# Kernel tuning notes

Hardware: AMD Instinct MI355X
Metric: run time of the kernel (lower is better)

## Reference

```python
import jax, jax.numpy as jnp
import numpy as np

NUM_GRAPHS = 512


def setup_inputs() -> dict:
    key = jax.random.key(0)
    ks = jax.random.split(key, 16)
    N, E = 50000, 800000
    x = jax.random.normal(ks[0], (N, 3), dtype=jnp.float32)
    edge_index = jax.random.randint(ks[1], (2, E), 0, N, dtype=jnp.int64)
    batch = jnp.sort(jax.random.randint(ks[2], (N,), 0, NUM_GRAPHS, dtype=jnp.int64))

    def glorot(k, shape):
        fan_in, fan_out = shape
        lim = (6.0 / (fan_in + fan_out)) ** 0.5
        return jax.random.uniform(k, shape, jnp.float32, -lim, lim)

    return {
        "x": x, "edge_index": edge_index, "batch": batch,
        "W1": glorot(ks[3], (3, 32)),   "b1": jnp.zeros((32,), jnp.float32),
        "W2": glorot(ks[4], (32, 64)),  "b2": jnp.zeros((64,), jnp.float32),
        "W3": glorot(ks[5], (64, 128)), "b3": jnp.zeros((128,), jnp.float32),
        "Wf1": glorot(ks[6], (128, 32)), "bf1": jnp.zeros((32,), jnp.float32),
        "Wf2": glorot(ks[7], (32, 4)),   "bf2": jnp.zeros((4,), jnp.float32),
    }


def _gcn_conv(x, src, dst, norm, W, b, N):
    # GCNConv: h = x W, then symmetric-normalized aggregation, then bias.
    h = x @ W                                   # [N, out]
    msg = h[src] * norm[:, None]                # [E+N, out] gathered edge messages
    out = jax.ops.segment_sum(msg, dst, num_segments=N)
    return out + b


def reference(x, edge_index, batch, W1, b1, W2, b2, W3, b3, Wf1, bf1, Wf2, bf2):
    N = x.shape[0]
    loops = jnp.arange(N, dtype=edge_index.dtype)
    src = jnp.concatenate([edge_index[0], loops])   # add self-loops (GCNConv default)
    dst = jnp.concatenate([edge_index[1], loops])
    # symmetric normalization deg^-1/2[src] * deg^-1/2[dst], deg counted on dst
    deg = jax.ops.segment_sum(jnp.ones_like(dst, dtype=x.dtype), dst, num_segments=N)
    dinv = jnp.where(deg > 0, jax.lax.rsqrt(deg), 0.0)
    norm = dinv[src] * dinv[dst]                    # [E+N]

    h = jax.nn.relu(_gcn_conv(x, src, dst, norm, W1, b1, N))
    h = jax.nn.relu(_gcn_conv(h, src, dst, norm, W2, b2, N))
    h = jax.nn.relu(_gcn_conv(h, src, dst, norm, W3, b3, N))

    # global mean pool over graphs
    sums = jax.ops.segment_sum(h, batch, num_segments=NUM_GRAPHS)
    cnts = jax.ops.segment_sum(jnp.ones((N,), h.dtype), batch, num_segments=NUM_GRAPHS)
    pooled = sums / jnp.maximum(cnts, 1.0)[:, None]   # [G, 128]

    z = jax.nn.relu(pooled @ Wf1 + bf1)
    return z @ Wf2 + bf2                              # [G, 4]
```

## Files before the change

### kernel.cpp

```cpp
#include <hip/hip_runtime.h>

#define NN 50000
#define NE 800000
#define NG 512
#define CAP 64
#define NP 196
#define CH 3200
#define NCH 250

__global__ __launch_bounds__(256) void p1_hist_k(const int* __restrict__ dst,
                                                 int* __restrict__ Ht, int e) {
    __shared__ int lh[NP];
    int t = threadIdx.x, b = blockIdx.x;
    if (t < NP) lh[t] = 0;
    __syncthreads();
    int i0 = b * CH, i1 = min(e, i0 + CH);
    for (int i = i0 + t; i < i1; i += 256) atomicAdd(&lh[dst[i] >> 8], 1);
    __syncthreads();
    if (t < NP) Ht[t * NCH + b] = lh[t];
}

__global__ __launch_bounds__(256) void p2a_k(int* __restrict__ Ht, int* __restrict__ tot) {
    __shared__ int sh[256];
    int p = blockIdx.x, t = threadIdx.x;
    int v = (t < NCH) ? Ht[p * NCH + t] : 0;
    sh[t] = v;
    __syncthreads();
    for (int off = 1; off < 256; off <<= 1) {
        int x = (t >= off) ? sh[t - off] : 0;
        __syncthreads();
        sh[t] += x;
        __syncthreads();
    }
    if (t < NCH) Ht[p * NCH + t] = sh[t] - v;
    if (t == 255) tot[p] = sh[255];
}

__global__ __launch_bounds__(256) void p2b_k(const int* __restrict__ tot,
                                             int* __restrict__ start) {
    __shared__ int sh[256];
    int t = threadIdx.x;
    int v = (t < NP) ? tot[t] : 0;
    sh[t] = v;
    __syncthreads();
    for (int off = 1; off < 256; off <<= 1) {
        int x = (t >= off) ? sh[t - off] : 0;
        __syncthreads();
        sh[t] += x;
        __syncthreads();
    }
    if (t < NP) start[t] = sh[t] - v;
    if (t == 255) start[NP] = sh[255];
}

__global__ __launch_bounds__(256) void p3_place_k(const int* __restrict__ src,
                                                  const int* __restrict__ dst,
                                                  const int* __restrict__ Ht,
                                                  const int* __restrict__ start,
                                                  int* __restrict__ pak, int e) {
    __shared__ int cur[NP];
    int t = threadIdx.x, b = blockIdx.x;
    if (t < NP) cur[t] = start[t] + Ht[t * NCH + b];
    __syncthreads();
    int i0 = b * CH, i1 = min(e, i0 + CH);
    for (int i = i0 + t; i < i1; i += 256) {
        int d = dst[i], s = src[i];
        int p = d >> 8, dl = d & 255;
        int pos = atomicAdd(&cur[p], 1);
        pak[pos] = s | (dl << 16);
    }
}

__global__ __launch_bounds__(256) void p4_build_k(const int* __restrict__ pak,
                                                   const int* __restrict__ start,
                                                   const float* __restrict__ x,
                                                   int* __restrict__ fill,
                                                   float* __restrict__ dinv,
                                                   float* __restrict__ xs,
                                                   int* __restrict__ eidx, int n) {
    __shared__ int lh[256], curn[256];
    int p = blockIdx.x, t = threadIdx.x;
    lh[t] = 0;
    curn[t] = 0;
    __syncthreads();
    int s0 = start[p], s1 = start[p + 1];
    for (int i = s0 + t; i < s1; i += 256) atomicAdd(&lh[pak[i] >> 16], 1);
    __syncthreads();
    int node = p * 256 + t;
    if (node < n) {
        int dg = lh[t];
        fill[node] = dg;
        float d = rsqrtf((float)(dg + 1));
        dinv[node] = d;
        float4 v;
        v.x = x[node * 3 + 0] * d;
        v.y = x[node * 3 + 1] * d;
        v.z = x[node * 3 + 2] * d;
        v.w = 0.0f;
        *(float4*)(xs + (size_t)node * 4) = v;
    }
    __syncthreads();
    for (int i = s0 + t; i < s1; i += 256) {
        int w = pak[i];
        int dl = w >> 16, s = w & 0xFFFF;
        int pos = atomicAdd(&curn[dl], 1) & (CAP - 1);
        eidx[(size_t)(p * 256 + dl) * CAP + pos] = s;
    }
}

__global__ __launch_bounds__(256) void fused_l1_k(
    const int* __restrict__ deg, const int* __restrict__ eidx,
    const float* __restrict__ xs, const float* __restrict__ W1,
    const float* __restrict__ b1, const float* __restrict__ dinv,
    float* __restrict__ A2, int n) {
    __shared__ float act[64][4];
    int t = threadIdx.x;
    int node0 = blockIdx.x * 64;
    {
        int node = node0 + (t >> 2);
        int f = t & 3;
        if (node < n) {
            int e1 = deg[node];
            const int* __restrict__ eb = eidx + node * CAP;
            float acc = xs[(size_t)node * 4 + f];
            int e = 0;
            for (; e + 4 <= e1; e += 4) {
                int4 s = *(const int4*)(eb + e);
                float v0 = xs[(size_t)s.x * 4 + f];
                float v1 = xs[(size_t)s.y * 4 + f];
                float v2 = xs[(size_t)s.z * 4 + f];
                float v3 = xs[(size_t)s.w * 4 + f];
                acc += (v0 + v1) + (v2 + v3);
            }
            for (; e < e1; ++e) acc += xs[(size_t)eb[e] * 4 + f];
            act[t >> 2][f] = acc;
        }
    }
    __syncthreads();
    int f = t & 31;
    int nl0 = t >> 5;
#pragma unroll
    for (int i = 0; i < 8; ++i) {
        int nl = nl0 + i * 8;
        int node = node0 + nl;
        if (node < n) {
            float acc = act[nl][0] * W1[f] + act[nl][1] * W1[32 + f] + act[nl][2] * W1[64 + f];
            float s = dinv[node];
            A2[(size_t)node * 32 + f] = fmaxf(fmaf(s, acc, b1[f]), 0.0f) * s;
        }
    }
}

template <int F>
__global__ __launch_bounds__(256) void gather4_k(const int* __restrict__ deg,
                                                 const int* __restrict__ eidx,
                                                 const float* __restrict__ A,
                                                 float* __restrict__ B, int n) {
    constexpr int FV = F / 4;
    constexpr int NPB = 256 / FV;
    int t = threadIdx.x;
    int node = blockIdx.x * NPB + t / FV;
    int j = (t % FV) * 4;
    if (node >= n) return;
    int e1 = deg[node];
    const int* __restrict__ eb = eidx + node * CAP;
    const float* __restrict__ Aj = A + j;
    float4 a0 = *(const float4*)(Aj + (size_t)node * F);
    float4 a1 = make_float4(0.f, 0.f, 0.f, 0.f);
    float4 a2 = make_float4(0.f, 0.f, 0.f, 0.f);
    float4 a3 = make_float4(0.f, 0.f, 0.f, 0.f);
    int e = 0;
    for (; e + 16 <= e1; e += 16) {
        int4 sa = *(const int4*)(eb + e);
        int4 sb = *(const int4*)(eb + e + 4);
        int4 sc = *(const int4*)(eb + e + 8);
        int4 sd = *(const int4*)(eb + e + 12);
        float4 v0 = *(const float4*)(Aj + (size_t)sa.x * F);
        float4 v1 = *(const float4*)(Aj + (size_t)sa.y * F);
        float4 v2 = *(const float4*)(Aj + (size_t)sa.z * F);
        float4 v3 = *(const float4*)(Aj + (size_t)sa.w * F);
        float4 v4 = *(const float4*)(Aj + (size_t)sb.x * F);
        float4 v5 = *(const float4*)(Aj + (size_t)sb.y * F);
        float4 v6 = *(const float4*)(Aj + (size_t)sb.z * F);
        float4 v7 = *(const float4*)(Aj + (size_t)sb.w * F);
        float4 v8 = *(const float4*)(Aj + (size_t)sc.x * F);
        float4 v9 = *(const float4*)(Aj + (size_t)sc.y * F);
        float4 va = *(const float4*)(Aj + (size_t)sc.z * F);
        float4 vb = *(const float4*)(Aj + (size_t)sc.w * F);
        float4 vc = *(const float4*)(Aj + (size_t)sd.x * F);
        float4 vd = *(const float4*)(Aj + (size_t)sd.y * F);
        float4 ve = *(const float4*)(Aj + (size_t)sd.z * F);
        float4 vf = *(const float4*)(Aj + (size_t)sd.w * F);
        a0.x += (v0.x + v1.x) + (v2.x + v3.x);
        a0.y += (v0.y + v1.y) + (v2.y + v3.y);
        a0.z += (v0.z + v1.z) + (v2.z + v3.z);
        a0.w += (v0.w + v1.w) + (v2.w + v3.w);
        a1.x += (v4.x + v5.x) + (v6.x + v7.x);
        a1.y += (v4.y + v5.y) + (v6.y + v7.y);
        a1.z += (v4.z + v5.z) + (v6.z + v7.z);
        a1.w += (v4.w + v5.w) + (v6.w + v7.w);
        a2.x += (v8.x + v9.x) + (va.x + vb.x);
        a2.y += (v8.y + v9.y) + (va.y + vb.y);
        a2.z += (v8.z + v9.z) + (va.z + vb.z);
        a2.w += (v8.w + v9.w) + (va.w + vb.w);
        a3.x += (vc.x + vd.x) + (ve.x + vf.x);
        a3.y += (vc.y + vd.y) + (ve.y + vf.y);
        a3.z += (vc.z + vd.z) + (ve.z + vf.z);
        a3.w += (vc.w + vd.w) + (ve.w + vf.w);
    }
    for (; e + 4 <= e1; e += 4) {
        int4 sa = *(const int4*)(eb + e);
        float4 v0 = *(const float4*)(Aj + (size_t)sa.x * F);
        float4 v1 = *(const float4*)(Aj + (size_t)sa.y * F);
        float4 v2 = *(const float4*)(Aj + (size_t)sa.z * F);
        float4 v3 = *(const float4*)(Aj + (size_t)sa.w * F);
        a1.x += (v0.x + v1.x) + (v2.x + v3.x);
        a1.y += (v0.y + v1.y) + (v2.y + v3.y);
        a1.z += (v0.z + v1.z) + (v2.z + v3.z);
        a1.w += (v0.w + v1.w) + (v2.w + v3.w);
    }
    for (; e < e1; ++e) {
        float4 v = *(const float4*)(Aj + (size_t)eb[e] * F);
        a0.x += v.x; a0.y += v.y; a0.z += v.z; a0.w += v.w;
    }
    a0.x += (a1.x + a2.x) + a3.x;
    a0.y += (a1.y + a2.y) + a3.y;
    a0.z += (a1.z + a2.z) + a3.z;
    a0.w += (a1.w + a2.w) + a3.w;
    *(float4*)(B + (size_t)node * F + j) = a0;
}

template <int Fin, int Fout, int NPB, bool SCALE_OUT>
__global__ __launch_bounds__(256) void mmB_k(
    const float* __restrict__ G, const float* __restrict__ W,
    const float* __restrict__ bias, const float* __restrict__ dinv,
    float* __restrict__ Aout, int n) {
    constexpr int FL = Fout / 4;
    constexpr int NGRP = 256 / FL;
    constexpr int NPT = NPB / NGRP;
    __shared__ float act[NPB][Fin];
    int t = threadIdx.x;
    int node0 = blockIdx.x * NPB;
    constexpr int TOT4 = NPB * Fin / 4;
    const float4* __restrict__ G4 = (const float4*)(G + (size_t)node0 * Fin);
    float4* act4 = (float4*)&act[0][0];
    for (int i = t; i < TOT4; i += 256) {
        int nl = i / (Fin / 4);
        float4 v = make_float4(0.f, 0.f, 0.f, 0.f);
        if (node0 + nl < n) v = G4[i];
        act4[i] = v;
    }
    __syncthreads();
    int f4 = (t % FL) * 4;
    int nlbase = (t / FL) * NPT;
    float4 acc[NPT];
#pragma unroll
    for (int i = 0; i < NPT; ++i) acc[i] = make_float4(0.f, 0.f, 0.f, 0.f);
    for (int k = 0; k < Fin; k += 4) {
        float4 a[NPT];
#pragma unroll
        for (int i = 0; i < NPT; ++i) a[i] = *(const float4*)&act[nlbase + i][k];
#pragma unroll
        for (int kk = 0; kk < 4; ++kk) {
            float4 w = *(const float4*)(W + (size_t)(k + kk) * Fout + f4);
#pragma unroll
            for (int i = 0; i < NPT; ++i) {
                float av = (&a[i].x)[kk];
                acc[i].x = fmaf(av, w.x, acc[i].x);
                acc[i].y = fmaf(av, w.y, acc[i].y);
                acc[i].z = fmaf(av, w.z, acc[i].z);
                acc[i].w = fmaf(av, w.w, acc[i].w);
            }
        }
    }
    float4 bv = *(const float4*)(bias + f4);
#pragma unroll
    for (int i = 0; i < NPT; ++i) {
        int node = node0 + nlbase + i;
        if (node < n) {
            float s = dinv[node];
            float4 o;
            o.x = fmaxf(fmaf(s, acc[i].x, bv.x), 0.0f);
            o.y = fmaxf(fmaf(s, acc[i].y, bv.y), 0.0f);
            o.z = fmaxf(fmaf(s, acc[i].z, bv.z), 0.0f);
            o.w = fmaxf(fmaf(s, acc[i].w, bv.w), 0.0f);
            if (SCALE_OUT) { o.x *= s; o.y *= s; o.z *= s; o.w *= s; }
            *(float4*)(Aout + (size_t)node * Fout + f4) = o;
        }
    }
}

__device__ __forceinline__ int lbound_d(const int* __restrict__ a, int n, int key) {
    int lo = 0, hi = n;
    while (lo < hi) {
        int m = (lo + hi) >> 1;
        if (a[m] < key) lo = m + 1; else hi = m;
    }
    return lo;
}

__global__ __launch_bounds__(128) void poolhead_k(
    const float* __restrict__ H, const int* __restrict__ batch,
    const float* __restrict__ Wf1, const float* __restrict__ bf1,
    const float* __restrict__ Wf2, const float* __restrict__ bf2,
    float* __restrict__ out, int n) {
    __shared__ int bnd[2];
    __shared__ float pm[128];
    __shared__ float z[32];
    int g = blockIdx.x, t = threadIdx.x;
    if (t == 0) bnd[0] = lbound_d(batch, n, g);
    if (t == 1) bnd[1] = lbound_d(batch, n, g + 1);
    __syncthreads();
    int lo = bnd[0], hi = bnd[1];
    float s0 = 0.f, s1 = 0.f, s2 = 0.f, s3 = 0.f;
    int i = lo;
    for (; i + 4 <= hi; i += 4) {
        s0 += H[(size_t)i * 128 + t];
        s1 += H[(size_t)(i + 1) * 128 + t];
        s2 += H[(size_t)(i + 2) * 128 + t];
        s3 += H[(size_t)(i + 3) * 128 + t];
    }
    for (; i < hi; ++i) s0 += H[(size_t)i * 128 + t];
    float c = (float)(hi - lo);
    c = fmaxf(c, 1.0f);
    pm[t] = ((s0 + s1) + (s2 + s3)) / c;
    __syncthreads();
    if (t < 32) {
        float acc = bf1[t];
#pragma unroll 4
        for (int k = 0; k < 128; ++k) acc = fmaf(pm[k], Wf1[k * 32 + t], acc);
        z[t] = fmaxf(acc, 0.0f);
    }
    __syncthreads();
    if (t < 4) {
        float acc = bf2[t];
#pragma unroll
        for (int jj = 0; jj < 32; ++jj) acc = fmaf(z[jj], Wf2[jj * 4 + t], acc);
        out[g * 4 + t] = acc;
    }
}

extern "C" void kernel_launch(void* const* d_in, const int* in_sizes, int n_in,
                              void* d_out, int out_size, void* d_ws, size_t ws_size,
                              hipStream_t stream) {
    const float* x    = (const float*)d_in[0];
    const int*   ei   = (const int*)d_in[1];
    const int*   batch= (const int*)d_in[2];
    const float* W1   = (const float*)d_in[3];
    const float* b1   = (const float*)d_in[4];
    const float* W2   = (const float*)d_in[5];
    const float* b2   = (const float*)d_in[6];
    const float* W3   = (const float*)d_in[7];
    const float* b3   = (const float*)d_in[8];
    const float* Wf1  = (const float*)d_in[9];
    const float* bf1  = (const float*)d_in[10];
    const float* Wf2  = (const float*)d_in[11];
    const float* bf2  = (const float*)d_in[12];
    float* out = (float*)d_out;

    int*   fill   = (int*)d_ws;
    float* dinv   = (float*)(fill + NN);
    float* xs     = dinv + NN;
    float* A2     = xs + (size_t)NN * 4;
    float* A3     = A2 + (size_t)NN * 32;
    float* H3     = A3 + (size_t)NN * 64;
    float* G      = H3 + (size_t)NN * 128;
    int*   eidx   = (int*)(G + (size_t)NN * 64);

    int* pak   = (int*)G;
    int* Ht    = (int*)H3;
    int* tot   = Ht + NP * NCH;
    int* start = tot + 256;

    const int* src = ei;
    const int* dst = ei + NE;

    p1_hist_k<<<NCH, 256, 0, stream>>>(dst, Ht, NE);
    p2a_k<<<NP, 256, 0, stream>>>(Ht, tot);
    p2b_k<<<1, 256, 0, stream>>>(tot, start);
    p3_place_k<<<NCH, 256, 0, stream>>>(src, dst, Ht, start, pak, NE);
    p4_build_k<<<NP, 256, 0, stream>>>(pak, start, x, fill, dinv, xs, eidx, NN);

    fused_l1_k<<<(NN + 63) / 64, 256, 0, stream>>>(fill, eidx, xs, W1, b1, dinv, A2, NN);

    gather4_k<32><<<(NN + 31) / 32, 256, 0, stream>>>(fill, eidx, A2, G, NN);
    mmB_k<32, 64, 32, true><<<(NN + 31) / 32, 256, 0, stream>>>(G, W2, b2, dinv, A3, NN);

    gather4_k<64><<<(NN + 15) / 16, 256, 0, stream>>>(fill, eidx, A3, G, NN);
    mmB_k<64, 128, 32, false><<<(NN + 31) / 32, 256, 0, stream>>>(G, W3, b3, dinv, H3, NN);

    poolhead_k<<<NG, 128, 0, stream>>>(H3, batch, Wf1, bf1, Wf2, bf2, out, NN);
}
```

Before: 222.8 us.

## Merge prefix-scan kernels, vectorize edge loads, and widen pooling block

Accumulates per-partition totals with atomics in the histogram kernel, so the separate global scan kernel is dropped. Each partition block now computes its own start offset by reducing the totals that precede it, and folds that offset into Ht so the placement kernel no longer reads start. Edge src/dst are loaded as int4 in the histogram and placement kernels, and the pooling kernel uses 256 threads that split node rows across two halves. This saves one launch and some memory traffic, but adds a memset and a redundant per-block reduction over the totals.

```diff
diff --git a/kernel.cpp b/kernel.cpp
--- a/kernel.cpp
+++ b/kernel.cpp
@@ -8,21 +8,43 @@
 #define CH 3200
 #define NCH 250
 
-__global__ __launch_bounds__(256) void p1_hist_k(const int* __restrict__ dst,
-                                                 int* __restrict__ Ht, int e) {
+__global__ __launch_bounds__(256) void p1_hist_k(const int4* __restrict__ dst4,
+                                                 int* __restrict__ Ht,
+                                                 int* __restrict__ tot) {
     __shared__ int lh[NP];
     int t = threadIdx.x, b = blockIdx.x;
     if (t < NP) lh[t] = 0;
     __syncthreads();
-    int i0 = b * CH, i1 = min(e, i0 + CH);
-    for (int i = i0 + t; i < i1; i += 256) atomicAdd(&lh[dst[i] >> 8], 1);
-    __syncthreads();
-    if (t < NP) Ht[t * NCH + b] = lh[t];
-}
-
-__global__ __launch_bounds__(256) void p2a_k(int* __restrict__ Ht, int* __restrict__ tot) {
+    int i0 = b * (CH / 4);
+    for (int i = i0 + t; i < i0 + CH / 4; i += 256) {
+        int4 d = dst4[i];
+        atomicAdd(&lh[d.x >> 8], 1);
+        atomicAdd(&lh[d.y >> 8], 1);
+        atomicAdd(&lh[d.z >> 8], 1);
+        atomicAdd(&lh[d.w >> 8], 1);
+    }
+    __syncthreads();
+    if (t < NP) {
+        Ht[t * NCH + b] = lh[t];
+        atomicAdd(&tot[t], lh[t]);
+    }
+}
+
+__global__ __launch_bounds__(256) void p2_k(int* __restrict__ Ht,
+                                            const int* __restrict__ tot,
+                                            int* __restrict__ start) {
     __shared__ int sh[256];
     int p = blockIdx.x, t = threadIdx.x;
+    sh[t] = (t < p) ? tot[t] : 0;
+    __syncthreads();
+    for (int off = 128; off > 0; off >>= 1) {
+        if (t < off) sh[t] += sh[t + off];
+        __syncthreads();
+    }
+    int start_p = sh[0];
+    __syncthreads();
+    if (t == 0) start[p] = start_p;
+    if (p == 0 && t == 1) start[NP] = NE;
     int v = (t < NCH) ? Ht[p * NCH + t] : 0;
     sh[t] = v;
     __syncthreads();
@@ -32,42 +54,26 @@
         sh[t] += x;
         __syncthreads();
     }
-    if (t < NCH) Ht[p * NCH + t] = sh[t] - v;
-    if (t == 255) tot[p] = sh[255];
-}
-
-__global__ __launch_bounds__(256) void p2b_k(const int* __restrict__ tot,
-                                             int* __restrict__ start) {
-    __shared__ int sh[256];
-    int t = threadIdx.x;
-    int v = (t < NP) ? tot[t] : 0;
-    sh[t] = v;
-    __syncthreads();
-    for (int off = 1; off < 256; off <<= 1) {
-        int x = (t >= off) ? sh[t - off] : 0;
-        __syncthreads();
-        sh[t] += x;
-        __syncthreads();
-    }
-    if (t < NP) start[t] = sh[t] - v;
-    if (t == 255) start[NP] = sh[255];
-}
-
-__global__ __launch_bounds__(256) void p3_place_k(const int* __restrict__ src,
-                                                  const int* __restrict__ dst,
+    if (t < NCH) Ht[p * NCH + t] = start_p + sh[t] - v;
+}
+
+__global__ __launch_bounds__(256) void p3_place_k(const int4* __restrict__ src4,
+                                                  const int4* __restrict__ dst4,
                                                   const int* __restrict__ Ht,
-                                                  const int* __restrict__ start,
-                                                  int* __restrict__ pak, int e) {
+                                                  int* __restrict__ pak) {
     __shared__ int cur[NP];
     int t = threadIdx.x, b = blockIdx.x;
-    if (t < NP) cur[t] = start[t] + Ht[t * NCH + b];
-    __syncthreads();
-    int i0 = b * CH, i1 = min(e, i0 + CH);
-    for (int i = i0 + t; i < i1; i += 256) {
-        int d = dst[i], s = src[i];
-        int p = d >> 8, dl = d & 255;
-        int pos = atomicAdd(&cur[p], 1);
-        pak[pos] = s | (dl << 16);
+    if (t < NP) cur[t] = Ht[t * NCH + b];
+    __syncthreads();
+    int i0 = b * (CH / 4);
+    for (int i = i0 + t; i < i0 + CH / 4; i += 256) {
+        int4 d = dst4[i];
+        int4 s = src4[i];
+        int pos;
+        pos = atomicAdd(&cur[d.x >> 8], 1); pak[pos] = s.x | ((d.x & 255) << 16);
+        pos = atomicAdd(&cur[d.y >> 8], 1); pak[pos] = s.y | ((d.y & 255) << 16);
+        pos = atomicAdd(&cur[d.z >> 8], 1); pak[pos] = s.z | ((d.z & 255) << 16);
+        pos = atomicAdd(&cur[d.w >> 8], 1); pak[pos] = s.w | ((d.w & 255) << 16);
     }
 }
 
@@ -299,36 +305,38 @@
     return lo;
 }
 
-__global__ __launch_bounds__(128) void poolhead_k(
+__global__ __launch_bounds__(256) void poolhead_k(
     const float* __restrict__ H, const int* __restrict__ batch,
     const float* __restrict__ Wf1, const float* __restrict__ bf1,
     const float* __restrict__ Wf2, const float* __restrict__ bf2,
     float* __restrict__ out, int n) {
     __shared__ int bnd[2];
-    __shared__ float pm[128];
+    __shared__ float pm2[2][128];
     __shared__ float z[32];
     int g = blockIdx.x, t = threadIdx.x;
     if (t == 0) bnd[0] = lbound_d(batch, n, g);
     if (t == 1) bnd[1] = lbound_d(batch, n, g + 1);
     __syncthreads();
     int lo = bnd[0], hi = bnd[1];
-    float s0 = 0.f, s1 = 0.f, s2 = 0.f, s3 = 0.f;
-    int i = lo;
-    for (; i + 4 <= hi; i += 4) {
-        s0 += H[(size_t)i * 128 + t];
-        s1 += H[(size_t)(i + 1) * 128 + t];
-        s2 += H[(size_t)(i + 2) * 128 + t];
-        s3 += H[(size_t)(i + 3) * 128 + t];
-    }
-    for (; i < hi; ++i) s0 += H[(size_t)i * 128 + t];
-    float c = (float)(hi - lo);
-    c = fmaxf(c, 1.0f);
-    pm[t] = ((s0 + s1) + (s2 + s3)) / c;
+    int f = t & 127, r = t >> 7;
+    float s0 = 0.f, s1 = 0.f;
+    int i = lo + r;
+    for (; i + 2 < hi; i += 4) {
+        s0 += H[(size_t)i * 128 + f];
+        s1 += H[(size_t)(i + 2) * 128 + f];
+    }
+    if (i < hi) s0 += H[(size_t)i * 128 + f];
+    pm2[r][f] = s0 + s1;
+    __syncthreads();
+    if (t < 128) {
+        float c = fmaxf((float)(hi - lo), 1.0f);
+        pm2[0][t] = (pm2[0][t] + pm2[1][t]) / c;
+    }
     __syncthreads();
     if (t < 32) {
         float acc = bf1[t];
 #pragma unroll 4
-        for (int k = 0; k < 128; ++k) acc = fmaf(pm[k], Wf1[k * 32 + t], acc);
+        for (int k = 0; k < 128; ++k) acc = fmaf(pm2[0][k], Wf1[k * 32 + t], acc);
         z[t] = fmaxf(acc, 0.0f);
     }
     __syncthreads();
@@ -370,15 +378,15 @@
     int* pak   = (int*)G;
     int* Ht    = (int*)H3;
     int* tot   = Ht + NP * NCH;
-    int* start = tot + 256;
-
-    const int* src = ei;
-    const int* dst = ei + NE;
-
-    p1_hist_k<<<NCH, 256, 0, stream>>>(dst, Ht, NE);
-    p2a_k<<<NP, 256, 0, stream>>>(Ht, tot);
-    p2b_k<<<1, 256, 0, stream>>>(tot, start);
-    p3_place_k<<<NCH, 256, 0, stream>>>(src, dst, Ht, start, pak, NE);
+    int* start = tot + NP;
+
+    const int4* src4 = (const int4*)ei;
+    const int4* dst4 = (const int4*)(ei + NE);
+
+    hipMemsetAsync(tot, 0, NP * 4, stream);
+    p1_hist_k<<<NCH, 256, 0, stream>>>(dst4, Ht, tot);
+    p2_k<<<NP, 256, 0, stream>>>(Ht, tot, start);
+    p3_place_k<<<NCH, 256, 0, stream>>>(src4, dst4, Ht, pak);
     p4_build_k<<<NP, 256, 0, stream>>>(pak, start, x, fill, dinv, xs, eidx, NN);
 
     fused_l1_k<<<(NN + 63) / 64, 256, 0, stream>>>(fill, eidx, xs, W1, b1, dinv, A2, NN);
@@ -389,5 +397,5 @@
     gather4_k<64><<<(NN + 15) / 16, 256, 0, stream>>>(fill, eidx, A3, G, NN);
     mmB_k<64, 128, 32, false><<<(NN + 31) / 32, 256, 0, stream>>>(G, W3, b3, dinv, H3, NN);
 
-    poolhead_k<<<NG, 128, 0, stream>>>(H3, batch, Wf1, bf1, Wf2, bf2, out, NN);
-}
+    poolhead_k<<<NG, 256, 0, stream>>>(H3, batch, Wf1, bf1, Wf2, bf2, out, NN);
+}
```

Result: no change. 224.5 us (+0.7%).
